# Performance work log

Hardware: AMD Instinct MI355X
Metric: run time of the kernel (lower is better)

The kernel has to match this reference:

```python
import jax, jax.numpy as jnp
import numpy as np

NEG_SLOPE = 0.2


def gat_conv(x, edge_index, W, a_src, a_dst, b):
    # PyG GATConv (heads=1, add_self_loops=True, concat -> out_channels)
    N = x.shape[0]
    h = x @ W                                   # [N, F_out]
    loops = jnp.arange(N, dtype=edge_index.dtype)
    src = jnp.concatenate([edge_index[0], loops])   # message sources (x_j)
    dst = jnp.concatenate([edge_index[1], loops])   # message targets (x_i)
    # attention logits: e = LeakyReLU(a_src . h_j + a_dst . h_i)
    alpha_s = h @ a_src                          # [N]
    alpha_d = h @ a_dst                          # [N]
    e = jax.nn.leaky_relu(alpha_s[src] + alpha_d[dst], NEG_SLOPE)  # [E+N]
    # segment softmax over incoming edges of each dst node
    m = jax.ops.segment_max(e, dst, num_segments=N)
    e = jnp.exp(e - m[dst])
    denom = jax.ops.segment_sum(e, dst, num_segments=N)
    alpha = e / denom[dst]                       # self-loops guarantee denom > 0
    # weighted scatter-sum aggregation
    out = jax.ops.segment_sum(alpha[:, None] * h[src], dst, num_segments=N)
    return out + b


def setup_inputs() -> dict:
    key = jax.random.key(0)
    ks = jax.random.split(key, 10)
    N, E, F_in, H, F_out = 100000, 3200000, 54, 16, 16
    x = jax.random.normal(ks[0], (N, F_in), dtype=jnp.float32)
    edge_index = jax.random.randint(ks[1], (2, E), 0, N, dtype=jnp.int64)
    s1 = 1.0 / np.sqrt(F_in)
    s2 = 1.0 / np.sqrt(H)
    return {
        "x": x,
        "edge_index": edge_index,
        "W1": jax.random.uniform(ks[2], (F_in, H), jnp.float32, -s1, s1),
        "a1_src": jax.random.uniform(ks[3], (H,), jnp.float32, -s2, s2),
        "a1_dst": jax.random.uniform(ks[4], (H,), jnp.float32, -s2, s2),
        "b1": jnp.zeros((H,), jnp.float32),
        "W2": jax.random.uniform(ks[5], (H, F_out), jnp.float32, -s2, s2),
        "a2_src": jax.random.uniform(ks[6], (F_out,), jnp.float32, -0.25, 0.25),
        "a2_dst": jax.random.uniform(ks[7], (F_out,), jnp.float32, -0.25, 0.25),
        "b2": jnp.zeros((F_out,), jnp.float32),
    }


def reference(x, edge_index, W1, a1_src, a1_dst, b1, W2, a2_src, a2_dst, b2):
    h = gat_conv(x, edge_index, W1, a1_src, a1_dst, b1)
    h = jax.nn.elu(h)
    # dropout p=0.5 is identity in eval mode
    out = gat_conv(h, edge_index, W2, a2_src, a2_dst, b2)
    return out
```

## Files before the change

### kernel.cpp

```cpp
#include <hip/hip_runtime.h>
#include <hip/hip_bf16.h>

typedef __hip_bfloat16 bf16;

static constexpr int N_NODES = 100000;
static constexpr int N_EDGES = 3200000;
static constexpr int F_IN    = 54;
static constexpr int F_HID   = 16;

static constexpr int BSHIFT    = 7;
static constexpr int BNODES    = 128;
static constexpr int NBUCK     = (N_NODES + BNODES - 1) / BNODES;
static constexpr int CAP_B     = 5120;
static constexpr int BIN_CHUNK = 4096;
static constexpr int BTHR      = 512;
static constexpr int EPT       = BIN_CHUNK / BTHR;
static constexpr int GRDB      = (N_EDGES + BIN_CHUNK - 1) / BIN_CHUNK;
static constexpr int GRDN_F    = (N_NODES + BTHR - 1) / BTHR;
static constexpr int HELD      = CAP_B / 512;

static constexpr size_t WS_FLAGS  = 0;
static constexpr size_t WS_ADST   = 4;
static constexpr size_t WS_ADST2  = 100004;
static constexpr size_t WS_BCNT   = 200004;
static constexpr size_t WS_ASRC1  = 201028;
static constexpr size_t WS_ASRC2  = 301028;
static constexpr size_t WS_HC1    = 401028;
static constexpr size_t WS_RCNT   = 1201028;
static constexpr size_t WS_RBEG   = 1301028;
static constexpr size_t WS_HC2    = 2001028;
static constexpr size_t WS_BEDGES = 3601028;
static constexpr size_t WS_SRCS   = 7604868;
static constexpr size_t WS_BUCKET_END = WS_SRCS + (size_t)NBUCK * CAP_B;
static constexpr size_t WS_FB_DEN     = 3601028;
static constexpr size_t WS_FB_AS      = 3701028;
static constexpr size_t WS_ATOMIC_END = 3801028;

__device__ __forceinline__ float lrelu(float v) { return fmaxf(v, 0.2f * v); }
__device__ __forceinline__ float loadf(const void* p, int i, bool f32) {
    return f32 ? ((const float*)p)[i] : __bfloat162float(((const bf16*)p)[i]);
}
__device__ __forceinline__ unsigned f2bf(float f) {
    unsigned u = __float_as_uint(f);
    return (u + 0x7FFFu + ((u >> 16) & 1u)) >> 16;
}
__device__ __forceinline__ float bflo(unsigned u) { return __uint_as_float(u << 16); }
__device__ __forceinline__ float bfhi(unsigned u) { return __uint_as_float(u & 0xFFFF0000u); }

__global__ __launch_bounds__(256) void k_probe0(
    const void* __restrict__ x, const void* __restrict__ ei,
    int* __restrict__ flags, int* __restrict__ bcnt)
{
    __shared__ int cnt, nz;
    const int t = threadIdx.x;
    if (t == 0) { cnt = 0; nz = 0; }
    __syncthreads();
    const unsigned u = ((const unsigned*)x)[t];
    if ((u & 0x7FFFu) >= 0x4800u) atomicAdd(&cnt, 1);
    if (t < 64) {
        if (((const unsigned*)ei)[2 * t + 1] != 0u) atomicAdd(&nz, 1);
    }
    for (int i = t; i < 1024; i += 256) bcnt[i] = 0;
    __syncthreads();
    if (t == 0) flags[0] = ((cnt >= 16) ? 1 : 0) | ((nz == 0) ? 2 : 0);
}

__global__ __launch_bounds__(512, 8) void k_binfeat(
    const void* __restrict__ ei, const void* __restrict__ x,
    const void* __restrict__ W1, const void* __restrict__ a_s,
    const void* __restrict__ a_d, const int* __restrict__ flags,
    int* __restrict__ bcnt, int* __restrict__ bedges,
    unsigned* __restrict__ hc, float* __restrict__ asrc, float* __restrict__ adst)
{
    __shared__ int   hist[NBUCK];
    __shared__ int   base[NBUCK];
    __shared__ float Wl[F_IN * F_HID];
    __shared__ float asl[F_HID];
    __shared__ float adl[F_HID];
    const int t = threadIdx.x;
    const bool f32 = flags[0] & 1;
    const bool i64 = flags[0] & 2;

    if (blockIdx.x < GRDB) {
        const int e0 = blockIdx.x * BIN_CHUNK;
        const int valid = min(BIN_CHUNK, N_EDGES - e0);
        for (int i = t; i < NBUCK; i += BTHR) hist[i] = 0;
        __syncthreads();
        int cval_r[EPT];
        int bkt_r[EPT];
#pragma unroll
        for (int q = 0; q < EPT; ++q) {
            const int idx = q * BTHR + t;
            const int e = e0 + idx;
            bkt_r[q] = -1;
            if (idx < valid) {
                int s, d;
                if (i64) {
                    s = ((const int*)ei)[2 * (size_t)e];
                    d = ((const int*)ei)[2 * ((size_t)N_EDGES + e)];
                } else {
                    s = ((const int*)ei)[e];
                    d = ((const int*)ei)[(size_t)N_EDGES + e];
                }
                bkt_r[q] = d >> BSHIFT;
                cval_r[q] = (s << BSHIFT) | (d & (BNODES - 1));
                atomicAdd(&hist[bkt_r[q]], 1);
            }
        }
        __syncthreads();
        for (int i = t; i < NBUCK; i += BTHR) {
            const int c = hist[i];
            base[i] = c ? atomicAdd(&bcnt[i], c) : 0;
            hist[i] = 0;
        }
        __syncthreads();
#pragma unroll
        for (int q = 0; q < EPT; ++q) {
            if (bkt_r[q] >= 0) {
                const int b = bkt_r[q];
                const int r = atomicAdd(&hist[b], 1);
                const int pos = base[b] + r;
                if (pos < CAP_B) bedges[(size_t)b * CAP_B + pos] = cval_r[q];
            }
        }
    } else {
        for (int i = t; i < F_IN * F_HID; i += BTHR) Wl[i] = loadf(W1, i, f32);
        if (t < F_HID) { asl[t] = loadf(a_s, t, f32); adl[t] = loadf(a_d, t, f32); }
        __syncthreads();
        const int node = (blockIdx.x - GRDB) * BTHR + t;
        if (node >= N_NODES) return;

        float h[F_HID];
#pragma unroll
        for (int k = 0; k < F_HID; ++k) h[k] = 0.f;
        if (f32) {
            const float2* xp = (const float2*)((const float*)x + (size_t)node * F_IN);
#pragma unroll
            for (int j = 0; j < F_IN / 2; ++j) {
                const float2 v = xp[j];
#pragma unroll
                for (int k = 0; k < F_HID; ++k) {
                    h[k] = fmaf(v.x, Wl[(2*j)   * F_HID + k], h[k]);
                    h[k] = fmaf(v.y, Wl[(2*j+1) * F_HID + k], h[k]);
                }
            }
        } else {
            const unsigned* xu = (const unsigned*)x + (size_t)node * (F_IN / 2);
#pragma unroll
            for (int j = 0; j < F_IN / 2; ++j) {
                const unsigned u = xu[j];
                const float v0 = __uint_as_float(u << 16);
                const float v1 = __uint_as_float(u & 0xFFFF0000u);
#pragma unroll
                for (int k = 0; k < F_HID; ++k) {
                    h[k] = fmaf(v0, Wl[(2*j)   * F_HID + k], h[k]);
                    h[k] = fmaf(v1, Wl[(2*j+1) * F_HID + k], h[k]);
                }
            }
        }
        float s = 0.f, d = 0.f;
#pragma unroll
        for (int k = 0; k < F_HID; ++k) { s = fmaf(h[k], asl[k], s); d = fmaf(h[k], adl[k], d); }
        asrc[node] = s;
        adst[node] = d;
        unsigned pk[8];
#pragma unroll
        for (int q = 0; q < 8; ++q) pk[q] = f2bf(h[2*q]) | (f2bf(h[2*q+1]) << 16);
        uint4* hb = (uint4*)(hc + ((size_t)node << 3));
        hb[0] = make_uint4(pk[0], pk[1], pk[2], pk[3]);
        hb[1] = make_uint4(pk[4], pk[5], pk[6], pk[7]);
    }
}

__device__ __forceinline__ void bucket_sort_lds(
    const int* __restrict__ bedges, const int* __restrict__ bcnt, int b, int t,
    int* hist, int* scanv, int* cur, int* srt)
{
    if (t < BNODES) hist[t] = 0;
    __syncthreads();
    const int cnt = min(bcnt[b], CAP_B);
    const int* cv = bedges + (size_t)b * CAP_B;
    int held[HELD];
#pragma unroll
    for (int q = 0; q < HELD; ++q) {
        const int e = t + q * 512;
        const int v = cv[e];
        held[q] = (e < cnt) ? v : -1;
    }
#pragma unroll
    for (int q = 0; q < HELD; ++q)
        if (held[q] >= 0) atomicAdd(&hist[held[q] & (BNODES - 1)], 1);
    __syncthreads();
    if (t < BNODES) scanv[t] = hist[t];
    __syncthreads();
#pragma unroll
    for (int off = 1; off < BNODES; off <<= 1) {
        const int v = (t < BNODES && t >= off) ? scanv[t - off] : 0;
        __syncthreads();
        if (t < BNODES) scanv[t] += v;
        __syncthreads();
    }
    if (t < BNODES) cur[t] = scanv[t] - hist[t];
    __syncthreads();
#pragma unroll
    for (int q = 0; q < HELD; ++q) {
        if (held[q] >= 0) {
            const int p  = held[q];
            const int r  = atomicAdd(&cur[p & (BNODES - 1)], 1);
            srt[r] = p >> BSHIFT;
        }
    }
    __syncthreads();
}

#define GATHER12(HCP, ASP)                                                     \
    for (; i + 12 <= n; i += 12) {                                             \
        const int s0 = sp[i+0], s1 = sp[i+1], s2_ = sp[i+2], s3 = sp[i+3];     \
        const int s4 = sp[i+4], s5 = sp[i+5], s6 = sp[i+6], s7 = sp[i+7];      \
        const int s8 = sp[i+8], s9 = sp[i+9], sa_ = sp[i+10], sb_ = sp[i+11];  \
        const uint2 v0 = *(const uint2*)(HCP + ((size_t)s0 << 3) + (k2 << 1)); \
        const uint2 v1 = *(const uint2*)(HCP + ((size_t)s1 << 3) + (k2 << 1)); \
        const uint2 v2 = *(const uint2*)(HCP + ((size_t)s2_ << 3) + (k2 << 1));\
        const uint2 v3 = *(const uint2*)(HCP + ((size_t)s3 << 3) + (k2 << 1)); \
        const uint2 v4 = *(const uint2*)(HCP + ((size_t)s4 << 3) + (k2 << 1)); \
        const uint2 v5 = *(const uint2*)(HCP + ((size_t)s5 << 3) + (k2 << 1)); \
        const uint2 v6 = *(const uint2*)(HCP + ((size_t)s6 << 3) + (k2 << 1)); \
        const uint2 v7 = *(const uint2*)(HCP + ((size_t)s7 << 3) + (k2 << 1)); \
        const uint2 v8 = *(const uint2*)(HCP + ((size_t)s8 << 3) + (k2 << 1)); \
        const uint2 v9 = *(const uint2*)(HCP + ((size_t)s9 << 3) + (k2 << 1)); \
        const uint2 va = *(const uint2*)(HCP + ((size_t)sa_ << 3) + (k2 << 1));\
        const uint2 vb = *(const uint2*)(HCP + ((size_t)sb_ << 3) + (k2 << 1));\
        const float x0 = ASP[s0], x1 = ASP[s1], x2 = ASP[s2_], x3 = ASP[s3];   \
        const float x4 = ASP[s4], x5 = ASP[s5], x6 = ASP[s6], x7 = ASP[s7];    \
        const float x8 = ASP[s8], x9 = ASP[s9], xa = ASP[sa_], xb = ASP[sb_];  \
        const float e0 = __expf(lrelu(x0 + adn));                              \
        const float e1 = __expf(lrelu(x1 + adn));                              \
        const float e2 = __expf(lrelu(x2 + adn));                              \
        const float e3 = __expf(lrelu(x3 + adn));                              \
        const float e4 = __expf(lrelu(x4 + adn));                              \
        const float e5 = __expf(lrelu(x5 + adn));                              \
        const float e6 = __expf(lrelu(x6 + adn));                              \
        const float e7 = __expf(lrelu(x7 + adn));                              \
        const float e8 = __expf(lrelu(x8 + adn));                              \
        const float e9 = __expf(lrelu(x9 + adn));                              \
        const float ea = __expf(lrelu(xa + adn));                              \
        const float eb = __expf(lrelu(xb + adn));                              \
        denom += ((e0 + e1 + e2) + (e3 + e4 + e5)) +                           \
                 ((e6 + e7 + e8) + (e9 + ea + eb));                            \
        a0 = fmaf(e0, bflo(v0.x), a0); a1 = fmaf(e0, bfhi(v0.x), a1);          \
        a2 = fmaf(e0, bflo(v0.y), a2); a3 = fmaf(e0, bfhi(v0.y), a3);          \
        a0 = fmaf(e1, bflo(v1.x), a0); a1 = fmaf(e1, bfhi(v1.x), a1);          \
        a2 = fmaf(e1, bflo(v1.y), a2); a3 = fmaf(e1, bfhi(v1.y), a3);          \
        a0 = fmaf(e2, bflo(v2.x), a0); a1 = fmaf(e2, bfhi(v2.x), a1);          \
        a2 = fmaf(e2, bflo(v2.y), a2); a3 = fmaf(e2, bfhi(v2.y), a3);          \
        a0 = fmaf(e3, bflo(v3.x), a0); a1 = fmaf(e3, bfhi(v3.x), a1);          \
        a2 = fmaf(e3, bflo(v3.y), a2); a3 = fmaf(e3, bfhi(v3.y), a3);          \
        a0 = fmaf(e4, bflo(v4.x), a0); a1 = fmaf(e4, bfhi(v4.x), a1);          \
        a2 = fmaf(e4, bflo(v4.y), a2); a3 = fmaf(e4, bfhi(v4.y), a3);          \
        a0 = fmaf(e5, bflo(v5.x), a0); a1 = fmaf(e5, bfhi(v5.x), a1);          \
        a2 = fmaf(e5, bflo(v5.y), a2); a3 = fmaf(e5, bfhi(v5.y), a3);          \
        a0 = fmaf(e6, bflo(v6.x), a0); a1 = fmaf(e6, bfhi(v6.x), a1);          \
        a2 = fmaf(e6, bflo(v6.y), a2); a3 = fmaf(e6, bfhi(v6.y), a3);          \
        a0 = fmaf(e7, bflo(v7.x), a0); a1 = fmaf(e7, bfhi(v7.x), a1);          \
        a2 = fmaf(e7, bflo(v7.y), a2); a3 = fmaf(e7, bfhi(v7.y), a3);          \
        a0 = fmaf(e8, bflo(v8.x), a0); a1 = fmaf(e8, bfhi(v8.x), a1);          \
        a2 = fmaf(e8, bflo(v8.y), a2); a3 = fmaf(e8, bfhi(v8.y), a3);          \
        a0 = fmaf(e9, bflo(v9.x), a0); a1 = fmaf(e9, bfhi(v9.x), a1);          \
        a2 = fmaf(e9, bflo(v9.y), a2); a3 = fmaf(e9, bfhi(v9.y), a3);          \
        a0 = fmaf(ea, bflo(va.x), a0); a1 = fmaf(ea, bfhi(va.x), a1);          \
        a2 = fmaf(ea, bflo(va.y), a2); a3 = fmaf(ea, bfhi(va.y), a3);          \
        a0 = fmaf(eb, bflo(vb.x), a0); a1 = fmaf(eb, bfhi(vb.x), a1);          \
        a2 = fmaf(eb, bflo(vb.y), a2); a3 = fmaf(eb, bfhi(vb.y), a3);          \
    }                                                                          \
    for (; i + 4 <= n; i += 4) {                                               \
        const int s0 = sp[i+0], s1 = sp[i+1], s2_ = sp[i+2], s3 = sp[i+3];     \
        const uint2 v0 = *(const uint2*)(HCP + ((size_t)s0 << 3) + (k2 << 1)); \
        const uint2 v1 = *(const uint2*)(HCP + ((size_t)s1 << 3) + (k2 << 1)); \
        const uint2 v2 = *(const uint2*)(HCP + ((size_t)s2_ << 3) + (k2 << 1));\
        const uint2 v3 = *(const uint2*)(HCP + ((size_t)s3 << 3) + (k2 << 1)); \
        const float x0 = ASP[s0], x1 = ASP[s1], x2 = ASP[s2_], x3 = ASP[s3];   \
        const float e0 = __expf(lrelu(x0 + adn));                              \
        const float e1 = __expf(lrelu(x1 + adn));                              \
        const float e2 = __expf(lrelu(x2 + adn));                              \
        const float e3 = __expf(lrelu(x3 + adn));                              \
        denom += (e0 + e1) + (e2 + e3);                                        \
        a0 = fmaf(e0, bflo(v0.x), a0); a1 = fmaf(e0, bfhi(v0.x), a1);          \
        a2 = fmaf(e0, bflo(v0.y), a2); a3 = fmaf(e0, bfhi(v0.y), a3);          \
        a0 = fmaf(e1, bflo(v1.x), a0); a1 = fmaf(e1, bfhi(v1.x), a1);          \
        a2 = fmaf(e1, bflo(v1.y), a2); a3 = fmaf(e1, bfhi(v1.y), a3);          \
        a0 = fmaf(e2, bflo(v2.x), a0); a1 = fmaf(e2, bfhi(v2.x), a1);          \
        a2 = fmaf(e2, bflo(v2.y), a2); a3 = fmaf(e2, bfhi(v2.y), a3);          \
        a0 = fmaf(e3, bflo(v3.x), a0); a1 = fmaf(e3, bfhi(v3.x), a1);          \
        a2 = fmaf(e3, bflo(v3.y), a2); a3 = fmaf(e3, bfhi(v3.y), a3);          \
    }                                                                          \
    for (; i < n; ++i) {                                                       \
        const int s = sp[i];                                                   \
        const uint2 v = *(const uint2*)(HCP + ((size_t)s << 3) + (k2 << 1));   \
        const float w = __expf(lrelu(ASP[s] + adn));                           \
        denom += w;                                                            \
        a0 = fmaf(w, bflo(v.x), a0); a1 = fmaf(w, bfhi(v.x), a1);              \
        a2 = fmaf(w, bflo(v.y), a2); a3 = fmaf(w, bfhi(v.y), a3);              \
    }

__global__ __launch_bounds__(512, 6) void k_agg1(
    const int* __restrict__ bcnt, const int* __restrict__ bedges,
    const float* __restrict__ asrc, const float* __restrict__ adst,
    const unsigned* __restrict__ hc,
    const void* __restrict__ b1, const void* __restrict__ W2,
    const void* __restrict__ a_s2, const void* __restrict__ a_d2,
    const int* __restrict__ flags,
    unsigned* __restrict__ hc2, float* __restrict__ asrc2, float* __restrict__ adst2,
    int* __restrict__ srcs_g, int* __restrict__ rowcnt_g, int* __restrict__ rowbeg_g)
{
    __shared__ float Wl[F_HID * F_HID];
    __shared__ float asl[F_HID], adl[F_HID], bl[F_HID];
    __shared__ float adL[BNODES], asL[BNODES];
    __shared__ int hist[BNODES], scanv[BNODES], cur[BNODES];
    __shared__ int srt[CAP_B];
    const bool f32 = flags[0] & 1;
    const int t = threadIdx.x;
    const int b = blockIdx.x;
    const int n0 = b << BSHIFT;
    if (t < F_HID * F_HID) Wl[t] = loadf(W2, t, f32);
    if (t < F_HID) {
        asl[t] = loadf(a_s2, t, f32);
        adl[t] = loadf(a_d2, t, f32);
        bl[t]  = loadf(b1, t, f32);
    }
    if (t < BNODES) {
        const int node = n0 + t;
        const bool ok = node < N_NODES;
        adL[t] = ok ? adst[node] : 0.f;
        asL[t] = ok ? asrc[node] : 0.f;
    }
    bucket_sort_lds(bedges, bcnt, b, t, hist, scanv, cur, srt);

    {
        const int cnt = min(bcnt[b], CAP_B);
        int* sg = srcs_g + (size_t)b * CAP_B;
        for (int i = t; i < cnt; i += 512) sg[i] = srt[i];
        if (t < BNODES) {
            const int node_ = n0 + t;
            if (node_ < N_NODES) {
                rowcnt_g[node_] = hist[t];
                rowbeg_g[node_] = scanv[t] - hist[t];
            }
        }
    }

    const int k2 = t & 3;
    const int g  = t >> 2;
    const int node = n0 + g;
    if (node < N_NODES) {
        const int K = k2 << 2;
        const float adn = adL[g];
        const uint2 us = *(const uint2*)(hc + ((size_t)node << 3) + (k2 << 1));
        const float w0 = __expf(lrelu(asL[g] + adn));
        float denom = w0;
        float a0 = w0 * bflo(us.x), a1 = w0 * bfhi(us.x);
        float a2 = w0 * bflo(us.y), a3 = w0 * bfhi(us.y);
        const int n = hist[g];
        const int* sp = srt + (scanv[g] - n);
        int i = 0;
        GATHER12(hc, asrc)
        const float inv = 1.f / denom;
        float z0 = a0 * inv + bl[K+0];
        float z1 = a1 * inv + bl[K+1];
        float z2 = a2 * inv + bl[K+2];
        float z3 = a3 * inv + bl[K+3];
        z0 = z0 > 0.f ? z0 : expm1f(z0);
        z1 = z1 > 0.f ? z1 : expm1f(z1);
        z2 = z2 > 0.f ? z2 : expm1f(z2);
        z3 = z3 > 0.f ? z3 : expm1f(z3);
        float hh0 = 0.f, hh1 = 0.f, hh2 = 0.f, hh3 = 0.f;
#pragma unroll
        for (int jl = 0; jl < 4; ++jl) {
            const float zj0 = __shfl(z0, jl, 4);
            const float zj1 = __shfl(z1, jl, 4);
            const float zj2 = __shfl(z2, jl, 4);
            const float zj3 = __shfl(z3, jl, 4);
            const int jb = jl << 2;
            hh0 = fmaf(zj0, Wl[(jb+0)*F_HID + K+0], hh0);
            hh1 = fmaf(zj0, Wl[(jb+0)*F_HID + K+1], hh1);
            hh2 = fmaf(zj0, Wl[(jb+0)*F_HID + K+2], hh2);
            hh3 = fmaf(zj0, Wl[(jb+0)*F_HID + K+3], hh3);
            hh0 = fmaf(zj1, Wl[(jb+1)*F_HID + K+0], hh0);
            hh1 = fmaf(zj1, Wl[(jb+1)*F_HID + K+1], hh1);
            hh2 = fmaf(zj1, Wl[(jb+1)*F_HID + K+2], hh2);
            hh3 = fmaf(zj1, Wl[(jb+1)*F_HID + K+3], hh3);
            hh0 = fmaf(zj2, Wl[(jb+2)*F_HID + K+0], hh0);
            hh1 = fmaf(zj2, Wl[(jb+2)*F_HID + K+1], hh1);
            hh2 = fmaf(zj2, Wl[(jb+2)*F_HID + K+2], hh2);
            hh3 = fmaf(zj2, Wl[(jb+2)*F_HID + K+3], hh3);
            hh0 = fmaf(zj3, Wl[(jb+3)*F_HID + K+0], hh0);
            hh1 = fmaf(zj3, Wl[(jb+3)*F_HID + K+1], hh1);
            hh2 = fmaf(zj3, Wl[(jb+3)*F_HID + K+2], hh2);
            hh3 = fmaf(zj3, Wl[(jb+3)*F_HID + K+3], hh3);
        }
        float s2 = hh0*asl[K+0] + hh1*asl[K+1] + hh2*asl[K+2] + hh3*asl[K+3];
        float d2 = hh0*adl[K+0] + hh1*adl[K+1] + hh2*adl[K+2] + hh3*adl[K+3];
        s2 += __shfl_xor(s2, 1, 4); s2 += __shfl_xor(s2, 2, 4);
        d2 += __shfl_xor(d2, 1, 4); d2 += __shfl_xor(d2, 2, 4);
        uint2 w;
        w.x = f2bf(hh0) | (f2bf(hh1) << 16);
        w.y = f2bf(hh2) | (f2bf(hh3) << 16);
        *(uint2*)(hc2 + ((size_t)node << 3) + (k2 << 1)) = w;
        if (k2 == 0) { asrc2[node] = s2; adst2[node] = d2; }
    }
}

__global__ __launch_bounds__(512, 6) void k_agg2(
    const int* __restrict__ bcnt, const int* __restrict__ srcs_g,
    const int* __restrict__ rowcnt_g, const int* __restrict__ rowbeg_g,
    const float* __restrict__ asrc, const float* __restrict__ adst,
    const unsigned* __restrict__ hc,
    const void* __restrict__ b2, const int* __restrict__ flags,
    float* __restrict__ outp)
{
    __shared__ float bl[F_HID];
    __shared__ float adL[BNODES], asL[BNODES];
    __shared__ int histL[BNODES], begL[BNODES];
    __shared__ int srt[CAP_B];
    const bool f32 = flags[0] & 1;
    const int t = threadIdx.x;
    const int b = blockIdx.x;
    const int n0 = b << BSHIFT;
    if (t < F_HID) bl[t] = loadf(b2, t, f32);
    if (t < BNODES) {
        const int node_ = n0 + t;
        const bool ok = node_ < N_NODES;
        adL[t]  = ok ? adst[node_] : 0.f;
        asL[t]  = ok ? asrc[node_] : 0.f;
        histL[t] = ok ? rowcnt_g[node_] : 0;
        begL[t]  = ok ? rowbeg_g[node_] : 0;
    }
    const int cnt = min(bcnt[b], CAP_B);
    const int* sg = srcs_g + (size_t)b * CAP_B;
    for (int i = t; i < cnt; i += 512) srt[i] = sg[i];
    __syncthreads();

    const int k2 = t & 3;
    const int g  = t >> 2;
    const int node = n0 + g;
    if (node < N_NODES) {
        const int K = k2 << 2;
        const float adn = adL[g];
        const uint2 us = *(const uint2*)(hc + ((size_t)node << 3) + (k2 << 1));
        const float w0 = __expf(lrelu(asL[g] + adn));
        float denom = w0;
        float a0 = w0 * bflo(us.x), a1 = w0 * bfhi(us.x);
        float a2 = w0 * bflo(us.y), a3 = w0 * bfhi(us.y);
        const int n = histL[g];
        const int* sp = srt + begL[g];
        int i = 0;
        GATHER12(hc, asrc)
        const float inv = 1.f / denom;
        float4 o;
        o.x = a0 * inv + bl[K+0];
        o.y = a1 * inv + bl[K+1];
        o.z = a2 * inv + bl[K+2];
        o.w = a3 * inv + bl[K+3];
        *(float4*)(outp + ((size_t)node << 4) + K) = o;
    }
}

__global__ __launch_bounds__(256) void k_feat1(
    const void* __restrict__ x, const void* __restrict__ W1,
    const void* __restrict__ a_s, const void* __restrict__ a_d,
    const int* __restrict__ flags,
    float* __restrict__ hbuf, float* __restrict__ asrc, float* __restrict__ adst)
{
    const bool f32 = flags[0] & 1;
    __shared__ float Wl[F_IN * F_HID];
    __shared__ float asl[F_HID];
    __shared__ float adl[F_HID];
    const int t = threadIdx.x;
    for (int i = t; i < F_IN * F_HID; i += 256) Wl[i] = loadf(W1, i, f32);
    if (t < F_HID) { asl[t] = loadf(a_s, t, f32); adl[t] = loadf(a_d, t, f32); }
    __syncthreads();
    const int node = blockIdx.x * 256 + t;
    if (node >= N_NODES) return;
    float h[F_HID];
#pragma unroll
    for (int k = 0; k < F_HID; ++k) h[k] = 0.f;
    if (f32) {
        const float2* xp = (const float2*)((const float*)x + (size_t)node * F_IN);
#pragma unroll
        for (int j = 0; j < F_IN / 2; ++j) {
            const float2 v = xp[j];
#pragma unroll
            for (int k = 0; k < F_HID; ++k) {
                h[k] = fmaf(v.x, Wl[(2*j)   * F_HID + k], h[k]);
                h[k] = fmaf(v.y, Wl[(2*j+1) * F_HID + k], h[k]);
            }
        }
    } else {
        const unsigned* xu = (const unsigned*)x + (size_t)node * (F_IN / 2);
#pragma unroll
        for (int j = 0; j < F_IN / 2; ++j) {
            const unsigned u = xu[j];
            const float v0 = __uint_as_float(u << 16);
            const float v1 = __uint_as_float(u & 0xFFFF0000u);
#pragma unroll
            for (int k = 0; k < F_HID; ++k) {
                h[k] = fmaf(v0, Wl[(2*j)   * F_HID + k], h[k]);
                h[k] = fmaf(v1, Wl[(2*j+1) * F_HID + k], h[k]);
            }
        }
    }
    float s = 0.f, d = 0.f;
#pragma unroll
    for (int k = 0; k < F_HID; ++k) { s = fmaf(h[k], asl[k], s); d = fmaf(h[k], adl[k], d); }
    asrc[node] = s; adst[node] = d;
    float4* hb = (float4*)(hbuf + (size_t)node * F_HID);
#pragma unroll
    for (int q = 0; q < 4; ++q)
        hb[q] = make_float4(h[4*q], h[4*q+1], h[4*q+2], h[4*q+3]);
}

__global__ __launch_bounds__(256) void k_selfinit(
    const float* __restrict__ asrc, const float* __restrict__ adst,
    const float* __restrict__ h, float* __restrict__ denom, float* __restrict__ acc)
{
    const int t = blockIdx.x * 256 + threadIdx.x;
    if (t >= N_NODES * F_HID) return;
    const int n = t >> 4;
    const float w0 = __expf(lrelu(asrc[n] + adst[n]));
    if ((t & 15) == 0) denom[n] = w0;
    acc[t] = w0 * h[t];
}

__global__ __launch_bounds__(256) void k_edge(
    const void* __restrict__ ei, const int* __restrict__ flags,
    const float* __restrict__ asrc, const float* __restrict__ adst,
    const float* __restrict__ hbuf,
    float* __restrict__ denom, float* __restrict__ acc)
{
    const int e = blockIdx.x * 256 + threadIdx.x;
    if (e >= N_EDGES) return;
    int s, d;
    if (flags[0] & 2) {
        const long long* e64 = (const long long*)ei;
        s = (int)e64[e]; d = (int)e64[(size_t)N_EDGES + e];
    } else {
        const int* e32 = (const int*)ei;
        s = e32[e]; d = e32[(size_t)N_EDGES + e];
    }
    const float w = __expf(lrelu(asrc[s] + adst[d]));
    atomicAdd(&denom[d], w);
    const float4* hs = (const float4*)(hbuf + (size_t)s * F_HID);
    float* ad = acc + (size_t)d * F_HID;
#pragma unroll
    for (int q = 0; q < 4; ++q) {
        const float4 hv = hs[q];
        atomicAdd(ad + 4*q + 0, w * hv.x);
        atomicAdd(ad + 4*q + 1, w * hv.y);
        atomicAdd(ad + 4*q + 2, w * hv.z);
        atomicAdd(ad + 4*q + 3, w * hv.w);
    }
}

__global__ __launch_bounds__(256) void k_div_elu(
    float* __restrict__ acc, const float* __restrict__ denom,
    const void* __restrict__ b1, const int* __restrict__ flags)
{
    const bool f32 = flags[0] & 1;
    const int t = blockIdx.x * 256 + threadIdx.x;
    if (t >= N_NODES * F_HID) return;
    const float v = acc[t] / denom[t >> 4] + loadf(b1, t & 15, f32);
    acc[t] = v > 0.f ? v : expm1f(v);
}

__global__ __launch_bounds__(256) void k_mid(
    const float* __restrict__ z,
    const void* __restrict__ W2, const void* __restrict__ a_s2,
    const void* __restrict__ a_d2, const int* __restrict__ flags,
    float* __restrict__ h2, float* __restrict__ asrc, float* __restrict__ adst)
{
    const bool f32 = flags[0] & 1;
    __shared__ float Wl[F_HID * F_HID];
    __shared__ float asl[F_HID];
    __shared__ float adl[F_HID];
    const int t = threadIdx.x;
    if (t < F_HID * F_HID) Wl[t] = loadf(W2, t, f32);
    if (t < F_HID) { asl[t] = loadf(a_s2, t, f32); adl[t] = loadf(a_d2, t, f32); }
    __syncthreads();
    const int node = blockIdx.x * 256 + t;
    if (node >= N_NODES) return;
    float zr[F_HID];
    const float4* zi = (const float4*)(z + (size_t)node * F_HID);
#pragma unroll
    for (int q = 0; q < 4; ++q) {
        const float4 zv = zi[q];
        zr[4*q+0]=zv.x; zr[4*q+1]=zv.y; zr[4*q+2]=zv.z; zr[4*q+3]=zv.w;
    }
    float h[F_HID];
#pragma unroll
    for (int k = 0; k < F_HID; ++k) h[k] = 0.f;
#pragma unroll
    for (int j = 0; j < F_HID; ++j) {
        const float zv = zr[j];
#pragma unroll
        for (int k = 0; k < F_HID; ++k) h[k] = fmaf(zv, Wl[j * F_HID + k], h[k]);
    }
    float s = 0.f, d = 0.f;
#pragma unroll
    for (int k = 0; k < F_HID; ++k) { s = fmaf(h[k], asl[k], s); d = fmaf(h[k], adl[k], d); }
    asrc[node] = s; adst[node] = d;
    float4* hb = (float4*)(h2 + (size_t)node * F_HID);
#pragma unroll
    for (int q = 0; q < 4; ++q)
        hb[q] = make_float4(h[4*q], h[4*q+1], h[4*q+2], h[4*q+3]);
}

__global__ __launch_bounds__(256) void k_out(
    const float* __restrict__ acc, const float* __restrict__ denom,
    const void* __restrict__ b2, const int* __restrict__ flags,
    float* __restrict__ out)
{
    const bool f32 = flags[0] & 1;
    const int t = blockIdx.x * 256 + threadIdx.x;
    if (t >= N_NODES * F_HID) return;
    out[t] = acc[t] / denom[t >> 4] + loadf(b2, t & 15, f32);
}

__global__ __launch_bounds__(256) void k_diag(float* __restrict__ out, float v)
{
    const int t = blockIdx.x * 256 + threadIdx.x;
    if (t < N_NODES * F_HID) out[t] = v;
}

extern "C" void kernel_launch(void* const* d_in, const int* in_sizes, int n_in,
                              void* d_out, int out_size, void* d_ws, size_t ws_size,
                              hipStream_t stream) {
    const void* x   = d_in[0];
    const void* ei  = d_in[1];
    const void* W1  = d_in[2];
    const void* a1s = d_in[3];
    const void* a1d = d_in[4];
    const void* b1  = d_in[5];
    const void* W2  = d_in[6];
    const void* a2s = d_in[7];
    const void* a2d = d_in[8];
    const void* b2  = d_in[9];
    float* out = (float*)d_out;

    float* ws = (float*)d_ws;
    int*      flags  = (int*)(ws + WS_FLAGS);
    float*    adst   = ws + WS_ADST;
    float*    adst2  = ws + WS_ADST2;
    int*      bcnt   = (int*)(ws + WS_BCNT);
    float*    asrc1  = ws + WS_ASRC1;
    float*    asrc2  = ws + WS_ASRC2;
    unsigned* hc1    = (unsigned*)(ws + WS_HC1);
    unsigned* hc2    = (unsigned*)(ws + WS_HC2);
    int*      rowcnt = (int*)(ws + WS_RCNT);
    int*      rowbeg = (int*)(ws + WS_RBEG);
    int*      bedges = (int*)(ws + WS_BEDGES);
    int*      srcs   = (int*)(ws + WS_SRCS);

    const dim3 blk(256);
    const dim3 grdN((N_NODES + 255) / 256);
    const dim3 grdE((N_EDGES + 255) / 256);
    const dim3 grdO((N_NODES * F_HID + 255) / 256);
    const dim3 grdBF(GRDB + GRDN_F);
    const dim3 grdB(NBUCK);

    if (ws_size >= WS_BUCKET_END * 4) {
        k_probe0 <<<dim3(1), blk, 0, stream>>>(x, ei, flags, bcnt);
        k_binfeat<<<grdBF, dim3(BTHR), 0, stream>>>(ei, x, W1, a1s, a1d, flags,
                                                    bcnt, bedges, hc1, asrc1, adst);
        k_agg1   <<<grdB, dim3(512), 0, stream>>>(bcnt, bedges, asrc1, adst, hc1,
                                                  b1, W2, a2s, a2d, flags,
                                                  hc2, asrc2, adst2,
                                                  srcs, rowcnt, rowbeg);
        k_agg2   <<<grdB, dim3(512), 0, stream>>>(bcnt, srcs, rowcnt, rowbeg,
                                                  asrc2, adst2, hc2,
                                                  b2, flags, out);
    } else if (ws_size >= WS_ATOMIC_END * 4) {
        float* fb_h   = ws + WS_HC1;
        float* fb_acc = ws + WS_HC2;
        float* fb_den = ws + WS_FB_DEN;
        float* fb_as  = ws + WS_FB_AS;
        float* fb_ad  = ws + WS_ADST;
        k_probe0 <<<dim3(1), blk, 0, stream>>>(x, ei, flags, bcnt);
        k_feat1  <<<grdN, blk, 0, stream>>>(x, W1, a1s, a1d, flags, fb_h, fb_as, fb_ad);
        k_selfinit<<<grdO, blk, 0, stream>>>(fb_as, fb_ad, fb_h, fb_den, fb_acc);
        k_edge   <<<grdE, blk, 0, stream>>>(ei, flags, fb_as, fb_ad, fb_h, fb_den, fb_acc);
        k_div_elu<<<grdO, blk, 0, stream>>>(fb_acc, fb_den, b1, flags);
        k_mid    <<<grdN, blk, 0, stream>>>(fb_acc, W2, a2s, a2d, flags, fb_h, fb_as, fb_ad);
        k_selfinit<<<grdO, blk, 0, stream>>>(fb_as, fb_ad, fb_h, fb_den, fb_acc);
        k_edge   <<<grdE, blk, 0, stream>>>(ei, flags, fb_as, fb_ad, fb_h, fb_den, fb_acc);
        k_out    <<<grdO, blk, 0, stream>>>(fb_acc, fb_den, b2, flags, out);
    } else {
        k_diag<<<grdO, blk, 0, stream>>>(out, (float)(ws_size >> 10));
    }
}
```

Before: 226.6 us.

## Split agg2 buckets across two 256-thread blocks and shrink gather unroll to 8

k_agg2 now launches two blocks per 128-node bucket, each handling 64 nodes with 256 threads and loading only its contiguous slice of the sorted source list into shared memory. The goal is more, smaller blocks for better occupancy and load balance. The gather macro used by both aggregation kernels is reduced from a 12-way unroll with a 4-way tail to a single 8-way unroll, which lowers register pressure but exposes fewer independent loads per iteration. A serial min/max scan by thread 0 and an extra barrier are added to find the slice bounds.

```diff
diff --git a/kernel.cpp b/kernel.cpp
--- a/kernel.cpp
+++ b/kernel.cpp
@@ -213,11 +213,10 @@
     __syncthreads();
 }
 
-#define GATHER12(HCP, ASP)                                                     \
-    for (; i + 12 <= n; i += 12) {                                             \
+#define GATHER8(HCP, ASP)                                                      \
+    for (; i + 8 <= n; i += 8) {                                               \
         const int s0 = sp[i+0], s1 = sp[i+1], s2_ = sp[i+2], s3 = sp[i+3];     \
         const int s4 = sp[i+4], s5 = sp[i+5], s6 = sp[i+6], s7 = sp[i+7];      \
-        const int s8 = sp[i+8], s9 = sp[i+9], sa_ = sp[i+10], sb_ = sp[i+11];  \
         const uint2 v0 = *(const uint2*)(HCP + ((size_t)s0 << 3) + (k2 << 1)); \
         const uint2 v1 = *(const uint2*)(HCP + ((size_t)s1 << 3) + (k2 << 1)); \
         const uint2 v2 = *(const uint2*)(HCP + ((size_t)s2_ << 3) + (k2 << 1));\
@@ -226,13 +225,8 @@
         const uint2 v5 = *(const uint2*)(HCP + ((size_t)s5 << 3) + (k2 << 1)); \
         const uint2 v6 = *(const uint2*)(HCP + ((size_t)s6 << 3) + (k2 << 1)); \
         const uint2 v7 = *(const uint2*)(HCP + ((size_t)s7 << 3) + (k2 << 1)); \
-        const uint2 v8 = *(const uint2*)(HCP + ((size_t)s8 << 3) + (k2 << 1)); \
-        const uint2 v9 = *(const uint2*)(HCP + ((size_t)s9 << 3) + (k2 << 1)); \
-        const uint2 va = *(const uint2*)(HCP + ((size_t)sa_ << 3) + (k2 << 1));\
-        const uint2 vb = *(const uint2*)(HCP + ((size_t)sb_ << 3) + (k2 << 1));\
         const float x0 = ASP[s0], x1 = ASP[s1], x2 = ASP[s2_], x3 = ASP[s3];   \
         const float x4 = ASP[s4], x5 = ASP[s5], x6 = ASP[s6], x7 = ASP[s7];    \
-        const float x8 = ASP[s8], x9 = ASP[s9], xa = ASP[sa_], xb = ASP[sb_];  \
         const float e0 = __expf(lrelu(x0 + adn));                              \
         const float e1 = __expf(lrelu(x1 + adn));                              \
         const float e2 = __expf(lrelu(x2 + adn));                              \
@@ -241,12 +235,7 @@
         const float e5 = __expf(lrelu(x5 + adn));                              \
         const float e6 = __expf(lrelu(x6 + adn));                              \
         const float e7 = __expf(lrelu(x7 + adn));                              \
-        const float e8 = __expf(lrelu(x8 + adn));                              \
-        const float e9 = __expf(lrelu(x9 + adn));                              \
-        const float ea = __expf(lrelu(xa + adn));                              \
-        const float eb = __expf(lrelu(xb + adn));                              \
-        denom += ((e0 + e1 + e2) + (e3 + e4 + e5)) +                           \
-                 ((e6 + e7 + e8) + (e9 + ea + eb));                            \
+        denom += (e0 + e1 + e2 + e3) + (e4 + e5 + e6 + e7);                    \
         a0 = fmaf(e0, bflo(v0.x), a0); a1 = fmaf(e0, bfhi(v0.x), a1);          \
         a2 = fmaf(e0, bflo(v0.y), a2); a3 = fmaf(e0, bfhi(v0.y), a3);          \
         a0 = fmaf(e1, bflo(v1.x), a0); a1 = fmaf(e1, bfhi(v1.x), a1);          \
@@ -263,35 +252,6 @@
         a2 = fmaf(e6, bflo(v6.y), a2); a3 = fmaf(e6, bfhi(v6.y), a3);          \
         a0 = fmaf(e7, bflo(v7.x), a0); a1 = fmaf(e7, bfhi(v7.x), a1);          \
         a2 = fmaf(e7, bflo(v7.y), a2); a3 = fmaf(e7, bfhi(v7.y), a3);          \
-        a0 = fmaf(e8, bflo(v8.x), a0); a1 = fmaf(e8, bfhi(v8.x), a1);          \
-        a2 = fmaf(e8, bflo(v8.y), a2); a3 = fmaf(e8, bfhi(v8.y), a3);          \
-        a0 = fmaf(e9, bflo(v9.x), a0); a1 = fmaf(e9, bfhi(v9.x), a1);          \
-        a2 = fmaf(e9, bflo(v9.y), a2); a3 = fmaf(e9, bfhi(v9.y), a3);          \
-        a0 = fmaf(ea, bflo(va.x), a0); a1 = fmaf(ea, bfhi(va.x), a1);          \
-        a2 = fmaf(ea, bflo(va.y), a2); a3 = fmaf(ea, bfhi(va.y), a3);          \
-        a0 = fmaf(eb, bflo(vb.x), a0); a1 = fmaf(eb, bfhi(vb.x), a1);          \
-        a2 = fmaf(eb, bflo(vb.y), a2); a3 = fmaf(eb, bfhi(vb.y), a3);          \
-    }                                                                          \
-    for (; i + 4 <= n; i += 4) {                                               \
-        const int s0 = sp[i+0], s1 = sp[i+1], s2_ = sp[i+2], s3 = sp[i+3];     \
-        const uint2 v0 = *(const uint2*)(HCP + ((size_t)s0 << 3) + (k2 << 1)); \
-        const uint2 v1 = *(const uint2*)(HCP + ((size_t)s1 << 3) + (k2 << 1)); \
-        const uint2 v2 = *(const uint2*)(HCP + ((size_t)s2_ << 3) + (k2 << 1));\
-        const uint2 v3 = *(const uint2*)(HCP + ((size_t)s3 << 3) + (k2 << 1)); \
-        const float x0 = ASP[s0], x1 = ASP[s1], x2 = ASP[s2_], x3 = ASP[s3];   \
-        const float e0 = __expf(lrelu(x0 + adn));                              \
-        const float e1 = __expf(lrelu(x1 + adn));                              \
-        const float e2 = __expf(lrelu(x2 + adn));                              \
-        const float e3 = __expf(lrelu(x3 + adn));                              \
-        denom += (e0 + e1) + (e2 + e3);                                        \
-        a0 = fmaf(e0, bflo(v0.x), a0); a1 = fmaf(e0, bfhi(v0.x), a1);          \
-        a2 = fmaf(e0, bflo(v0.y), a2); a3 = fmaf(e0, bfhi(v0.y), a3);          \
-        a0 = fmaf(e1, bflo(v1.x), a0); a1 = fmaf(e1, bfhi(v1.x), a1);          \
-        a2 = fmaf(e1, bflo(v1.y), a2); a3 = fmaf(e1, bfhi(v1.y), a3);          \
-        a0 = fmaf(e2, bflo(v2.x), a0); a1 = fmaf(e2, bfhi(v2.x), a1);          \
-        a2 = fmaf(e2, bflo(v2.y), a2); a3 = fmaf(e2, bfhi(v2.y), a3);          \
-        a0 = fmaf(e3, bflo(v3.x), a0); a1 = fmaf(e3, bfhi(v3.x), a1);          \
-        a2 = fmaf(e3, bflo(v3.y), a2); a3 = fmaf(e3, bfhi(v3.y), a3);          \
     }                                                                          \
     for (; i < n; ++i) {                                                       \
         const int s = sp[i];                                                   \
@@ -362,7 +322,7 @@
         const int n = hist[g];
         const int* sp = srt + (scanv[g] - n);
         int i = 0;
-        GATHER12(hc, asrc)
+        GATHER8(hc, asrc)
         const float inv = 1.f / denom;
         float z0 = a0 * inv + bl[K+0];
         float z1 = a1 * inv + bl[K+1];
@@ -409,7 +369,7 @@
     }
 }
 
-__global__ __launch_bounds__(512, 6) void k_agg2(
+__global__ __launch_bounds__(256, 8) void k_agg2(
     const int* __restrict__ bcnt, const int* __restrict__ srcs_g,
     const int* __restrict__ rowcnt_g, const int* __restrict__ rowbeg_g,
     const float* __restrict__ asrc, const float* __restrict__ adst,
@@ -418,15 +378,17 @@
     float* __restrict__ outp)
 {
     __shared__ float bl[F_HID];
-    __shared__ float adL[BNODES], asL[BNODES];
-    __shared__ int histL[BNODES], begL[BNODES];
-    __shared__ int srt[CAP_B];
+    __shared__ float adL[64], asL[64];
+    __shared__ int histL[64], begL[64];
+    __shared__ int srtL[CAP_B];
+    __shared__ int sh_beg0, sh_len;
     const bool f32 = flags[0] & 1;
     const int t = threadIdx.x;
-    const int b = blockIdx.x;
-    const int n0 = b << BSHIFT;
+    const int blk = blockIdx.x;
+    const int b = blk >> 1;
+    const int n0 = (b << BSHIFT) + ((blk & 1) << 6);
     if (t < F_HID) bl[t] = loadf(b2, t, f32);
-    if (t < BNODES) {
+    if (t < 64) {
         const int node_ = n0 + t;
         const bool ok = node_ < N_NODES;
         adL[t]  = ok ? adst[node_] : 0.f;
@@ -434,9 +396,24 @@
         histL[t] = ok ? rowcnt_g[node_] : 0;
         begL[t]  = ok ? rowbeg_g[node_] : 0;
     }
-    const int cnt = min(bcnt[b], CAP_B);
-    const int* sg = srcs_g + (size_t)b * CAP_B;
-    for (int i = t; i < cnt; i += 512) srt[i] = sg[i];
+    __syncthreads();
+    if (t == 0) {
+        int beg0 = 0x7FFFFFFF, endv = 0;
+        for (int g = 0; g < 64; ++g) {
+            if (n0 + g < N_NODES) {
+                beg0 = min(beg0, begL[g]);
+                endv = max(endv, begL[g] + histL[g]);
+            }
+        }
+        if (beg0 == 0x7FFFFFFF) { beg0 = 0; endv = 0; }
+        sh_beg0 = beg0;
+        sh_len  = endv - beg0;
+    }
+    __syncthreads();
+    const int beg0 = sh_beg0;
+    const int len  = sh_len;
+    const int* sg = srcs_g + (size_t)b * CAP_B + beg0;
+    for (int i = t; i < len; i += 256) srtL[i] = sg[i];
     __syncthreads();
 
     const int k2 = t & 3;
@@ -451,9 +428,9 @@
         float a0 = w0 * bflo(us.x), a1 = w0 * bfhi(us.x);
         float a2 = w0 * bflo(us.y), a3 = w0 * bfhi(us.y);
         const int n = histL[g];
-        const int* sp = srt + begL[g];
+        const int* sp = srtL + (begL[g] - beg0);
         int i = 0;
-        GATHER12(hc, asrc)
+        GATHER8(hc, asrc)
         const float inv = 1.f / denom;
         float4 o;
         o.x = a0 * inv + bl[K+0];
@@ -665,6 +642,7 @@
     const dim3 grdO((N_NODES * F_HID + 255) / 256);
     const dim3 grdBF(GRDB + GRDN_F);
     const dim3 grdB(NBUCK);
+    const dim3 grdB2(NBUCK * 2);
 
     if (ws_size >= WS_BUCKET_END * 4) {
         k_probe0 <<<dim3(1), blk, 0, stream>>>(x, ei, flags, bcnt);
@@ -674,9 +652,9 @@
                                                   b1, W2, a2s, a2d, flags,
                                                   hc2, asrc2, adst2,
                                                   srcs, rowcnt, rowbeg);
-        k_agg2   <<<grdB, dim3(512), 0, stream>>>(bcnt, srcs, rowcnt, rowbeg,
-                                                  asrc2, adst2, hc2,
-                                                  b2, flags, out);
+        k_agg2   <<<grdB2, dim3(256), 0, stream>>>(bcnt, srcs, rowcnt, rowbeg,
+                                                   asrc2, adst2, hc2,
+                                                   b2, flags, out);
     } else if (ws_size >= WS_ATOMIC_END * 4) {
         float* fb_h   = ws + WS_HC1;
         float* fb_acc = ws + WS_HC2;
```

Result: faster. 220.1 us (-2.8%).
